# Optimization experiments

Measured on AMD Instinct MI355X. Metric: run time of the kernel, lower is better.

Reference implementation:

```python
import jax, jax.numpy as jnp
import numpy as np
import math

N, C, E, K_TOP = 4096, 256, 131072, 32
NEG_SLOPE = 0.2  # GATConv default negative_slope


def _mlp(x, w1, b1, w2, b2):
    # Linear -> relu -> Linear (dropout is identity in eval mode)
    return jax.nn.relu(x @ w1 + b1) @ w2 + b2


def _gat_alpha(x, w, a_src, a_dst, src, dst, n):
    # PyG GATConv attention coefficients (heads=1), softmax over incoming edges per dst
    h = x @ w                                                   # [N,C]
    logits = jax.nn.leaky_relu((h @ a_src)[src] + (h @ a_dst)[dst], NEG_SLOPE)  # [E]
    m = jnp.full((n,), -jnp.inf, dtype=logits.dtype).at[dst].max(logits)
    e = jnp.exp(logits - m[dst])
    s = jax.ops.segment_sum(e, dst, num_segments=n)
    return e / s[dst]                                           # [E]


def _mha_w(x, wq, bq, wk, bk):
    # nn.MultiheadAttention attention weights, heads=1, unbatched [N,C] input
    q = x @ wq + bq
    k = x @ wk + bk
    return jax.nn.softmax((q @ k.T) * (1.0 / math.sqrt(C)), axis=-1)  # [N,N]


def _forward(ae, pe, se,
             ae_w1, ae_b1, ae_w2, ae_b2,
             pe_w1, pe_b1, pe_w2, pe_b2,
             se_w1, se_b1, se_w2, se_b2,
             ae_gw, ae_as, ae_ad,
             pe_gw, pe_as, pe_ad,
             se_gw, se_as, se_ad,
             ae_wq, ae_bq, ae_wk, ae_bk,
             pe_wq, pe_bq, pe_wk, pe_bk,
             se_wq, se_bq, se_wk, se_bk,
             a_l, b_l, c_l, a_g, b_g, c_g,
             w_local, w_global,
             edge_index, K):
    n = ae.shape[0]
    ae = _mlp(ae, ae_w1, ae_b1, ae_w2, ae_b2)
    pe = _mlp(pe, pe_w1, pe_b1, pe_w2, pe_b2)
    se = _mlp(se, se_w1, se_b1, se_w2, se_b2)

    src, dst = edge_index[0], edge_index[1]

    # ---- local branch: fused GAT attention coeffs -> weighted mean aggregation ----
    pa = _gat_alpha(pe, pe_gw, pe_as, pe_ad, src, dst, n)
    sa = _gat_alpha(se, se_gw, se_as, se_ad, src, dst, n)
    aa = _gat_alpha(ae, ae_gw, ae_as, ae_ad, src, dst, n)
    local_attn = a_l * pa + b_l * sa + c_l * aa                 # [E]
    msg = local_attn[:, None] * ae[src]                         # [E,C]
    summ = jax.ops.segment_sum(msg, dst, num_segments=n)
    cnt = jax.ops.segment_sum(jnp.ones((src.shape[0],), msg.dtype), dst, num_segments=n)
    out_local = summ / jnp.maximum(cnt, 1.0)[:, None]           # mean aggr

    # ---- global branch: dense self-attn maps + adj masking + per-column top-K ----
    pw = _mha_w(pe, pe_wq, pe_bq, pe_wk, pe_bk)                 # [N,N]
    sw = _mha_w(se, se_wq, se_bq, se_wk, se_bk)
    aw = _mha_w(ae, ae_wq, ae_bq, ae_wk, ae_bk)
    sample_attn = a_g * pw + b_g * sw
    adj = jnp.zeros((n, n), sample_attn.dtype).at[src, dst].add(1.0)
    sample_attn = jnp.where(adj > 0, jnp.zeros((), sample_attn.dtype), sample_attn)
    # torch topk(dim=1) on [1,N,N] == top-K along axis 0 (per column) of [N,N]
    _, idx = jax.lax.top_k(sample_attn.T, K)                    # [N,K] row indices per column
    maskT = jnp.zeros((n, n), sample_attn.dtype).at[jnp.arange(n)[:, None], idx].set(1.0)
    mask = maskT.T
    g_attn = (0.5 * a_g + 0.5 * b_g) * (sample_attn * mask) + c_g * (aw * mask)
    col = jnp.sum(g_attn, axis=0)                               # column sums (torch dim=1 on [1,N,N])
    g_attn = g_attn / col[None, :]
    out_global = g_attn @ ae                                    # [N,C]

    return out_local @ w_local + out_global @ w_global


def setup_inputs() -> dict:
    key = jax.random.key(0)
    it = iter(jax.random.split(key, 64))
    g = lambda shape, s=0.06: jax.random.normal(next(it), shape, dtype=jnp.float32) * s
    inp = {"ae": g((N, C), 1.0), "pe": g((N, C), 1.0), "se": g((N, C), 1.0)}
    for p in ("ae", "pe", "se"):
        inp[p + "_w1"] = g((C, 2 * C)); inp[p + "_b1"] = jnp.zeros((2 * C,), jnp.float32)
        inp[p + "_w2"] = g((2 * C, C)); inp[p + "_b2"] = jnp.zeros((C,), jnp.float32)
        inp[p + "_gw"] = g((C, C)); inp[p + "_as"] = g((C,)); inp[p + "_ad"] = g((C,))
        inp[p + "_wq"] = g((C, C)); inp[p + "_bq"] = jnp.zeros((C,), jnp.float32)
        inp[p + "_wk"] = g((C, C)); inp[p + "_bk"] = jnp.zeros((C,), jnp.float32)
    for s in ("a_l", "b_l", "c_l", "a_g", "b_g", "c_g"):
        inp[s] = jnp.float32(0.33)
    inp["w_local"] = g((C, C))
    inp["w_global"] = g((C, C))
    inp["edge_index"] = jax.random.randint(next(it), (2, E), 0, N, dtype=jnp.int32)
    inp["K"] = K_TOP
    return inp


def reference(ae, pe, se,
              ae_w1, ae_b1, ae_w2, ae_b2,
              pe_w1, pe_b1, pe_w2, pe_b2,
              se_w1, se_b1, se_w2, se_b2,
              ae_gw, ae_as, ae_ad,
              pe_gw, pe_as, pe_ad,
              se_gw, se_as, se_ad,
              ae_wq, ae_bq, ae_wk, ae_bk,
              pe_wq, pe_bq, pe_wk, pe_bk,
              se_wq, se_bq, se_wk, se_bk,
              a_l, b_l, c_l, a_g, b_g, c_g,
              w_local, w_global,
              edge_index, K):
    return _forward(ae, pe, se,
                    ae_w1, ae_b1, ae_w2, ae_b2,
                    pe_w1, pe_b1, pe_w2, pe_b2,
                    se_w1, se_b1, se_w2, se_b2,
                    ae_gw, ae_as, ae_ad,
                    pe_gw, pe_as, pe_ad,
                    se_gw, se_as, se_ad,
                    ae_wq, ae_bq, ae_wk, ae_bk,
                    pe_wq, pe_bq, pe_wk, pe_bk,
                    se_wq, se_bq, se_wk, se_bk,
                    a_l, b_l, c_l, a_g, b_g, c_g,
                    w_local, w_global,
                    edge_index, K)
```

## Files before the change

kernel.cpp:

```cpp
#include <hip/hip_runtime.h>

#define NN 4096
#define CC 256
#define EE 131072
#define KT 32

typedef unsigned short ushort_t;
typedef __attribute__((ext_vector_type(8))) short short8;
typedef __attribute__((ext_vector_type(4))) float float4v;

__device__ __forceinline__ ushort_t f2bf(float x) {
    union { float f; unsigned u; } a; a.f = x;
    unsigned r = (a.u + 0x7FFF + ((a.u >> 16) & 1)) >> 16;
    return (ushort_t)r;
}
__device__ __forceinline__ float bf2f(ushort_t b) {
    union { float f; unsigned u; } a; a.u = ((unsigned)b) << 16;
    return a.f;
}

constexpr size_t OFF_EPT  = 0;
constexpr size_t OFF_EST  = OFF_EPT + 16777216;
constexpr size_t OFF_LP   = OFF_EST + 16777216;
constexpr size_t OFF_LS   = OFF_LP + 4096;
constexpr size_t OFF_LA   = OFF_LS + 4096;
constexpr size_t OFF_ECNT = OFF_LA + 4096;
constexpr size_t OFF_GCNT = OFF_ECNT + 4096;
constexpr size_t OFF_ADJ  = OFF_GCNT + 4096;
constexpr size_t ZERO_END = OFF_ADJ + 524288;
constexpr size_t OFF_XM   = ZERO_END;
constexpr size_t OFF_QK   = OFF_XM + 3*1048576;
constexpr size_t OFF_WEXP = OFF_QK + 6*1048576;
constexpr size_t OFF_HS   = OFF_WEXP + 3*131072;
constexpr size_t OFF_HD   = OFF_HS + 12288;
constexpr size_t OFF_WSD  = OFF_HD + 12288;
constexpr size_t OFF_TKI  = OFF_WSD + 1536;
constexpr size_t OFF_TKV  = OFF_TKI + 131072;
constexpr size_t OFF_GN   = OFF_TKV + 131072;
constexpr size_t OFF_EOFF = OFF_GN + 131072;
constexpr size_t OFF_ECUR = OFF_EOFF + 4097;
constexpr size_t OFF_ELST = OFF_ECUR + 4096;
constexpr size_t OFF_GOFF = OFF_ELST + 131072;
constexpr size_t OFF_GCUR = OFF_GOFF + 4097;
constexpr size_t OFF_GLST = OFF_GCUR + 4096;
constexpr size_t OFF_WLT  = OFF_GLST + 131072;
constexpr size_t WS_FLOATS = OFF_WLT + 131072;

constexpr size_t SH_XINH = 0;
constexpr size_t SH_XINL = 3145728;
constexpr size_t SH_HIDH = 6291456;
constexpr size_t SH_HIDL = 12582912;
constexpr size_t SH_XMH  = 18874368;
constexpr size_t SH_XML  = 22020096;
constexpr size_t SH_WT   = 25165824;
constexpr size_t WT_BR   = 786432;

struct TArgs {
    const float* s[14]; ushort_t* h[14]; ushort_t* l[14];
    int nshift[14]; int total[14]; int kstride[14]; int koff[14];
};

__global__ __launch_bounds__(256)
void wtrans_k(TArgs a)
{
    int z = blockIdx.z;
    int idx = blockIdx.x * 256 + threadIdx.x;
    if (idx >= a.total[z]) return;
    int n = idx & ((1 << a.nshift[z]) - 1);
    int k = idx >> a.nshift[z];
    float v = a.s[z][idx];
    ushort_t hh = f2bf(v);
    size_t o = (size_t)n * a.kstride[z] + a.koff[z] + k;
    a.h[z][o] = hh;
    a.l[z][o] = f2bf(v - bf2f(hh));
}

__global__ __launch_bounds__(256)
void split3_k(const float* s0, const float* s1, const float* s2,
              ushort_t* hb, ushort_t* lb, size_t nper)
{
    int z = blockIdx.z;
    const float* s = (z == 0) ? s0 : (z == 1) ? s1 : s2;
    ushort_t* h = hb + (size_t)z * nper;
    ushort_t* l = lb + (size_t)z * nper;
    size_t i = (size_t)(blockIdx.x * 256 + threadIdx.x) * 4;
    float4 v = *(const float4*)(s + i);
    ushort_t h0 = f2bf(v.x), h1 = f2bf(v.y), h2 = f2bf(v.z), h3 = f2bf(v.w);
    ushort_t l0 = f2bf(v.x - bf2f(h0)), l1 = f2bf(v.y - bf2f(h1));
    ushort_t l2 = f2bf(v.z - bf2f(h2)), l3 = f2bf(v.w - bf2f(h3));
    uint2 hw, lw;
    hw.x = (unsigned)h0 | ((unsigned)h1 << 16); hw.y = (unsigned)h2 | ((unsigned)h3 << 16);
    lw.x = (unsigned)l0 | ((unsigned)l1 << 16); lw.y = (unsigned)l2 | ((unsigned)l3 << 16);
    *(uint2*)(h + i) = hw;
    *(uint2*)(l + i) = lw;
}

struct MArgs {
    const ushort_t* Ah[6]; const ushort_t* Al[6];
    const ushort_t* Bh[6]; const ushort_t* Bl[6];
    const float* bias[6];
    float* Cf[6]; ushort_t* Ch[6]; ushort_t* Cl[6];
};

template<int RELU>
__global__ __launch_bounds__(256)
void mgemm_k(MArgs a, int N, int K)
{
    __shared__ ushort_t SA[2][64 * 32];
    __shared__ ushort_t SB[2][64 * 32];

    const int z = blockIdx.z;
    const int t = threadIdx.x, wave = t >> 6, lane = t & 63;
    const int wi = wave & 1, wj = wave >> 1;
    const int lrow = lane & 15, lquad = lane >> 4;

    const ushort_t* src = (wave == 0) ? a.Ah[z] : (wave == 1) ? a.Al[z]
                        : (wave == 2) ? a.Bh[z] : a.Bl[z];
    ushort_t* dst = (wave == 0) ? &SA[0][0] : (wave == 1) ? &SA[1][0]
                  : (wave == 2) ? &SB[0][0] : &SB[1][0];
    const int rbase = ((wave < 2) ? blockIdx.x : blockIdx.y) * 64;
    const int sr = lane >> 2, sq = lane & 3;
    const int gsq = sq ^ ((sr >> 1) & 3);

    float4v acc[2][2] = {};

    for (int k0 = 0; k0 < K; k0 += 32) {
        #pragma unroll
        for (int it = 0; it < 4; ++it) {
            const ushort_t* g = src + (size_t)(rbase + it * 16 + sr) * K + k0 + gsq * 8;
            __builtin_amdgcn_global_load_lds(
                (const __attribute__((address_space(1))) void*)g,
                (__attribute__((address_space(3))) void*)(dst + it * 512),
                16, 0, 0);
        }
        __syncthreads();

        short8 fAh[2], fAl[2], fBh[2], fBl[2];
        #pragma unroll
        for (int mt = 0; mt < 2; ++mt) {
            int ra = wi * 32 + mt * 16 + lrow;
            int ca = (lquad ^ ((ra >> 1) & 3)) * 8;
            fAh[mt] = *(const short8*)&SA[0][ra * 32 + ca];
            fAl[mt] = *(const short8*)&SA[1][ra * 32 + ca];
        }
        #pragma unroll
        for (int nt = 0; nt < 2; ++nt) {
            int rb = wj * 32 + nt * 16 + lrow;
            int cb = (lquad ^ ((rb >> 1) & 3)) * 8;
            fBh[nt] = *(const short8*)&SB[0][rb * 32 + cb];
            fBl[nt] = *(const short8*)&SB[1][rb * 32 + cb];
        }
        #pragma unroll
        for (int mt = 0; mt < 2; ++mt)
            #pragma unroll
            for (int nt = 0; nt < 2; ++nt) {
                acc[mt][nt] = __builtin_amdgcn_mfma_f32_16x16x32_bf16(fAh[mt], fBh[nt], acc[mt][nt], 0, 0, 0);
                acc[mt][nt] = __builtin_amdgcn_mfma_f32_16x16x32_bf16(fAh[mt], fBl[nt], acc[mt][nt], 0, 0, 0);
                acc[mt][nt] = __builtin_amdgcn_mfma_f32_16x16x32_bf16(fAl[mt], fBh[nt], acc[mt][nt], 0, 0, 0);
            }
        __syncthreads();
    }

    const float* bias = a.bias[z];
    float* Cf = a.Cf[z];
    ushort_t* Ch = a.Ch[z]; ushort_t* Cl = a.Cl[z];
    const int i0w = blockIdx.x * 64 + wi * 32, j0w = blockIdx.y * 64 + wj * 32;
    #pragma unroll
    for (int mt = 0; mt < 2; ++mt) {
        const int ib = i0w + mt * 16 + lquad * 4;
        #pragma unroll
        for (int nt = 0; nt < 2; ++nt) {
            const int j = j0w + nt * 16 + lrow;
            float bj = bias ? bias[j] : 0.f;
            #pragma unroll
            for (int r = 0; r < 4; ++r) {
                float v = acc[mt][nt][r] + bj;
                if (RELU) v = fmaxf(v, 0.f);
                if (Cf) Cf[(size_t)(ib + r) * N + j] = v;
                if (Ch) {
                    ushort_t h = f2bf(v);
                    Ch[(size_t)(ib + r) * N + j] = h;
                    Cl[(size_t)(ib + r) * N + j] = f2bf(v - bf2f(h));
                }
            }
        }
    }
}

struct QArgs {
    const ushort_t* qh[3]; const ushort_t* ql[3];
    const ushort_t* kh[3]; const ushort_t* kl[3];
    float* ept[3]; float* rs[3];
};

__global__ __launch_bounds__(256)
void qk_mfma_k(QArgs a, float scale)
{
    __shared__ ushort_t SA[2][128 * 32];
    __shared__ ushort_t SB[2][128 * 32];

    const int z = blockIdx.z;
    const int t = threadIdx.x;
    const int wave = t >> 6, lane = t & 63;
    const int wi = wave & 1, wj = wave >> 1;
    const int i0w = blockIdx.x * 128 + wi * 64;
    const int j0w = blockIdx.y * 128 + wj * 64;
    const int lrow = lane & 15, lquad = lane >> 4;

    const ushort_t* src = (wave == 0) ? a.qh[z] : (wave == 1) ? a.ql[z]
                        : (wave == 2) ? a.kh[z] : a.kl[z];
    ushort_t* dst = (wave == 0) ? &SA[0][0] : (wave == 1) ? &SA[1][0]
                  : (wave == 2) ? &SB[0][0] : &SB[1][0];
    const int rbase = (wave < 2) ? blockIdx.x * 128 : blockIdx.y * 128;
    const int sr = lane >> 2, sq = lane & 3;
    const int gsq = sq ^ ((sr >> 1) & 3);

    float4v acc[4][4] = {};

    for (int k0 = 0; k0 < CC; k0 += 32) {
        #pragma unroll
        for (int it = 0; it < 8; ++it) {
            const ushort_t* g = src + (size_t)(rbase + it * 16 + sr) * CC + k0 + gsq * 8;
            __builtin_amdgcn_global_load_lds(
                (const __attribute__((address_space(1))) void*)g,
                (__attribute__((address_space(3))) void*)(dst + it * 512),
                16, 0, 0);
        }
        __syncthreads();

        short8 Ah[4], Al[4], Bh[4], Bl[4];
        #pragma unroll
        for (int mt = 0; mt < 4; ++mt) {
            int ra = wi * 64 + mt * 16 + lrow;
            int ca = (lquad ^ ((ra >> 1) & 3)) * 8;
            Ah[mt] = *(const short8*)&SA[0][ra * 32 + ca];
            Al[mt] = *(const short8*)&SA[1][ra * 32 + ca];
        }
        #pragma unroll
        for (int nt = 0; nt < 4; ++nt) {
            int rb = wj * 64 + nt * 16 + lrow;
            int cb = (lquad ^ ((rb >> 1) & 3)) * 8;
            Bh[nt] = *(const short8*)&SB[0][rb * 32 + cb];
            Bl[nt] = *(const short8*)&SB[1][rb * 32 + cb];
        }
        #pragma unroll
        for (int mt = 0; mt < 4; ++mt)
            #pragma unroll
            for (int nt = 0; nt < 4; ++nt) {
                acc[mt][nt] = __builtin_amdgcn_mfma_f32_16x16x32_bf16(Ah[mt], Bh[nt], acc[mt][nt], 0, 0, 0);
                acc[mt][nt] = __builtin_amdgcn_mfma_f32_16x16x32_bf16(Ah[mt], Bl[nt], acc[mt][nt], 0, 0, 0);
                acc[mt][nt] = __builtin_amdgcn_mfma_f32_16x16x32_bf16(Al[mt], Bh[nt], acc[mt][nt], 0, 0, 0);
            }
        __syncthreads();
    }

    float* ept = a.ept[z];
    float* rowsum = a.rs[z];
    #pragma unroll
    for (int mt = 0; mt < 4; ++mt) {
        const int ib = i0w + mt * 16 + lquad * 4;
        float part[4] = {0.f, 0.f, 0.f, 0.f};
        #pragma unroll
        for (int nt = 0; nt < 4; ++nt) {
            const int j = j0w + nt * 16 + lrow;
            float e0 = expf(acc[mt][nt][0] * scale);
            float e1 = expf(acc[mt][nt][1] * scale);
            float e2 = expf(acc[mt][nt][2] * scale);
            float e3 = expf(acc[mt][nt][3] * scale);
            part[0] += e0; part[1] += e1; part[2] += e2; part[3] += e3;
            if (ept)
                *(float4*)&ept[(size_t)j * NN + ib] = make_float4(e0, e1, e2, e3);
        }
        #pragma unroll
        for (int r = 0; r < 4; ++r) {
            float p = part[r];
            p += __shfl_xor(p, 1, 64);
            p += __shfl_xor(p, 2, 64);
            p += __shfl_xor(p, 4, 64);
            p += __shfl_xor(p, 8, 64);
            if (lrow == 0) atomicAdd(&rowsum[ib + r], p);
        }
    }
}

__global__ void invrows_k(float* __restrict__ lp, float* __restrict__ ls,
                          const float* agp, const float* bgp)
{
    int i = blockIdx.x * 256 + threadIdx.x;
    lp[i] = (*agp) / lp[i];
    ls[i] = (*bgp) / ls[i];
}

__global__ __launch_bounds__(256)
void gatvec_k(const float* g0, const float* g1, const float* g2,
              const float* v0, const float* v1, const float* v2,
              const float* v3, const float* v4, const float* v5,
              float* __restrict__ wsd)
{
    int b = blockIdx.x;
    const float* gw = (b < 2) ? g0 : (b < 4) ? g1 : g2;
    const float* av = (b == 0) ? v0 : (b == 1) ? v1 : (b == 2) ? v2
                    : (b == 3) ? v3 : (b == 4) ? v4 : v5;
    int tdx = threadIdx.x;
    float s = 0.f;
    for (int c = 0; c < CC; ++c) s += gw[(size_t)tdx * CC + c] * av[c];
    wsd[b * 256 + tdx] = s;
}

__global__ __launch_bounds__(256)
void hshd_k(const float* __restrict__ Xp, const float* __restrict__ Xs,
            const float* __restrict__ Xa, const float* __restrict__ wsd,
            float* __restrict__ hs, float* __restrict__ hd)
{
    int b = blockIdx.y, row = blockIdx.x, t = threadIdx.x;
    const float* X = (b == 0) ? Xp : (b == 1) ? Xs : Xa;
    float x = X[(size_t)row * CC + t];
    float p1 = x * wsd[b * 512 + t];
    float p2 = x * wsd[b * 512 + 256 + t];
    for (int off = 32; off; off >>= 1) {
        p1 += __shfl_down(p1, off, 64);
        p2 += __shfl_down(p2, off, 64);
    }
    __shared__ float s1[4], s2[4];
    if ((t & 63) == 0) { s1[t >> 6] = p1; s2[t >> 6] = p2; }
    __syncthreads();
    if (t == 0) {
        hs[b * NN + row] = s1[0] + s1[1] + s1[2] + s1[3];
        hd[b * NN + row] = s2[0] + s2[1] + s2[2] + s2[3];
    }
}

__global__ __launch_bounds__(256)
void edge_k(const int* __restrict__ ei, const float* __restrict__ hs,
            const float* __restrict__ hd, float* __restrict__ wexp,
            unsigned* __restrict__ bits, int* __restrict__ cnt)
{
    int e = blockIdx.x * 256 + threadIdx.x;
    int s = ei[e], d = ei[EE + e];
    #pragma unroll
    for (int b = 0; b < 3; ++b) {
        float l = hs[b * NN + s] + hd[b * NN + d];
        l = (l > 0.f) ? l : 0.2f * l;
        wexp[(size_t)b * EE + e] = expf(l);
    }
    size_t lin = (size_t)d * NN + s;
    atomicOr(&bits[lin >> 5], 1u << (lin & 31));
    atomicAdd(&cnt[d], 1);
}

__global__ void gcount_k(const int* __restrict__ tki, int* __restrict__ cnt)
{
    int p = blockIdx.x * 256 + threadIdx.x;
    atomicAdd(&cnt[tki[p]], 1);
}

__global__ __launch_bounds__(256)
void prefix_k(const int* __restrict__ cnt, int* __restrict__ off, int* __restrict__ cur)
{
    __shared__ int part[257];
    int t = threadIdx.x;
    int loc[16]; int s = 0;
    #pragma unroll
    for (int u = 0; u < 16; ++u) { loc[u] = s; s += cnt[t * 16 + u]; }
    part[t + 1] = s;
    if (t == 0) part[0] = 0;
    __syncthreads();
    if (t == 0) for (int i = 1; i <= 256; ++i) part[i] += part[i - 1];
    __syncthreads();
    int b = part[t];
    #pragma unroll
    for (int u = 0; u < 16; ++u) { off[t * 16 + u] = b + loc[u]; cur[t * 16 + u] = b + loc[u]; }
    if (t == 255) off[4096] = part[256];
}

__global__ void efill_k(const int* __restrict__ ei, int* __restrict__ cur,
                        int* __restrict__ lst)
{
    int e = blockIdx.x * 256 + threadIdx.x;
    int p = atomicAdd(&cur[ei[EE + e]], 1);
    lst[p] = e;
}

__global__ void gfill_k(const int* __restrict__ tki, int* __restrict__ cur,
                        int* __restrict__ lst)
{
    int p = blockIdx.x * 256 + threadIdx.x;
    int q = atomicAdd(&cur[tki[p]], 1);
    lst[q] = p;
}

__global__ __launch_bounds__(256)
void topk_k(const float* __restrict__ EPT, const float* __restrict__ EST,
            const float* __restrict__ ivp, const float* __restrict__ ivs,
            const unsigned* __restrict__ adjbits,
            int* __restrict__ tki, float* __restrict__ tkv)
{
    __shared__ unsigned lst[4][KT];
    const int j = blockIdx.x, t = threadIdx.x;
    const int w = t >> 6, lane = t & 63;
    const size_t base = (size_t)j * NN;

    unsigned keys[16], kmax = 0;
    #pragma unroll
    for (int u = 0; u < 16; ++u) {
        int i = w * 1024 + u * 64 + lane;
        float v = EPT[base + i] * ivp[i] + EST[base + i] * ivs[i];
        if ((adjbits[(base + i) >> 5] >> (i & 31)) & 1u) v = 0.f;
        union { float f; unsigned u32; } cv; cv.f = v;
        unsigned k = (cv.u32 & 0xFFFFFC00u) | (unsigned)(1023 - (i & 1023));
        keys[u] = k;
        kmax = k > kmax ? k : kmax;
    }

    for (int r = 0; r < KT; ++r) {
        unsigned k = kmax;
        #pragma unroll
        for (int off = 1; off < 64; off <<= 1) {
            unsigned o = __shfl_xor(k, off, 64);
            k = o > k ? o : k;
        }
        if (lane == 0) lst[w][r] = k;
        if (kmax == k) {
            kmax = 0;
            #pragma unroll
            for (int u = 0; u < 16; ++u) {
                if (keys[u] == k) keys[u] = 0;
                kmax = keys[u] > kmax ? keys[u] : kmax;
            }
        }
    }
    __syncthreads();

    if (t == 0) {
        unsigned h0 = lst[0][0], h1 = lst[1][0], h2 = lst[2][0], h3 = lst[3][0];
        int p0 = 0, p1 = 0, p2 = 0, p3 = 0;
        for (int r = 0; r < KT; ++r) {
            unsigned m01 = h0 > h1 ? h0 : h1;
            unsigned m23 = h2 > h3 ? h2 : h3;
            unsigned m = m01 > m23 ? m01 : m23;
            int wsel;
            if      (m == h0) { wsel = 0; ++p0; h0 = (p0 < KT) ? lst[0][p0] : 0; }
            else if (m == h1) { wsel = 1; ++p1; h1 = (p1 < KT) ? lst[1][p1] : 0; }
            else if (m == h2) { wsel = 2; ++p2; h2 = (p2 < KT) ? lst[2][p2] : 0; }
            else              { wsel = 3; ++p3; h3 = (p3 < KT) ? lst[3][p3] : 0; }
            union { unsigned u32; float f; } cv; cv.u32 = m & 0xFFFFFC00u;
            tkv[j * KT + r] = cv.f;
            tki[j * KT + r] = wsel * 1024 + 1023 - (int)(m & 0x3FFu);
        }
    }
}

__global__ __launch_bounds__(256)
void awcol_k(const ushort_t* __restrict__ qh, const ushort_t* __restrict__ ql,
             const ushort_t* __restrict__ kh, const ushort_t* __restrict__ kl,
             const float* __restrict__ La, const int* __restrict__ tki,
             const float* __restrict__ tkv,
             const float* agp, const float* bgp, const float* cgp,
             float* __restrict__ gn)
{
    __shared__ float kj[CC];
    __shared__ float gv[KT];
    __shared__ float cs_sh;
    int j = blockIdx.x, t = threadIdx.x;
    kj[t] = bf2f(kh[(size_t)j * CC + t]) + bf2f(kl[(size_t)j * CC + t]);
    __syncthreads();
    float hg = 0.5f * (*agp) + 0.5f * (*bgp), cg = *cgp;
    int wv = t >> 6, ln = t & 63;
    for (int k = wv; k < KT; k += 4) {
        int i = tki[j * KT + k];
        float p = 0.f;
        #pragma unroll
        for (int u = 0; u < 4; ++u) {
            int c = ln + u * 64;
            float q = bf2f(qh[(size_t)i * CC + c]) + bf2f(ql[(size_t)i * CC + c]);
            p += q * kj[c];
        }
        for (int off = 32; off; off >>= 1) p += __shfl_down(p, off, 64);
        if (ln == 0) {
            float aw = expf(p * 0.0625f) / La[i];
            gv[k] = hg * tkv[j * KT + k] + cg * aw;
        }
    }
    __syncthreads();
    if (t == 0) { float cs = 0.f; for (int k = 0; k < KT; ++k) cs += gv[k]; cs_sh = cs; }
    __syncthreads();
    if (t < KT) gn[j * KT + t] = gv[t] / cs_sh;
}

__global__ __launch_bounds__(256)
void lgather_k(const int* __restrict__ ei, const int* __restrict__ eoff,
               const int* __restrict__ elst,
               const float* __restrict__ wexp,
               const float* __restrict__ aem,
               const float* alp, const float* blp, const float* clp,
               ushort_t* __restrict__ outch, ushort_t* __restrict__ outcl)
{
    int wv = threadIdx.x >> 6, ln = threadIdx.x & 63;
    int d = blockIdx.x * 4 + wv;
    int beg = eoff[d], end = eoff[d + 1];

    float s1 = 0.f, s2 = 0.f, s3 = 0.f;
    for (int c = beg + ln; c < end; c += 64) {
        int e = elst[c];
        s1 += wexp[e];
        s2 += wexp[EE + e];
        s3 += wexp[2 * (size_t)EE + e];
    }
    #pragma unroll
    for (int off = 1; off < 64; off <<= 1) {
        s1 += __shfl_xor(s1, off, 64);
        s2 += __shfl_xor(s2, off, 64);
        s3 += __shfl_xor(s3, off, 64);
    }
    float i0 = (*alp) / s1, i1 = (*blp) / s2, i2 = (*clp) / s3;

    float4 acc = {0.f, 0.f, 0.f, 0.f};
    for (int c = beg; c < end; c += 64) {
        int n = min(64, end - c);
        int s = 0; float la = 0.f;
        if (ln < n) {
            int e = elst[c + ln];
            s = ei[e];
            la = i0 * wexp[e] + i1 * wexp[EE + e] + i2 * wexp[2 * (size_t)EE + e];
        }
        for (int u = 0; u < n; ++u) {
            float lau = __shfl(la, u, 64);
            int   su  = __shfl(s, u, 64);
            const float4 v = *(const float4*)&aem[(size_t)su * CC + ln * 4];
            acc.x += lau * v.x; acc.y += lau * v.y;
            acc.z += lau * v.z; acc.w += lau * v.w;
        }
    }
    float inv = 1.f / fmaxf((float)(end - beg), 1.f);
    acc.x *= inv; acc.y *= inv; acc.z *= inv; acc.w *= inv;
    ushort_t h0 = f2bf(acc.x), h1 = f2bf(acc.y), h2 = f2bf(acc.z), h3 = f2bf(acc.w);
    uint2 hw, lw;
    hw.x = (unsigned)h0 | ((unsigned)h1 << 16); hw.y = (unsigned)h2 | ((unsigned)h3 << 16);
    lw.x = (unsigned)f2bf(acc.x - bf2f(h0)) | ((unsigned)f2bf(acc.y - bf2f(h1)) << 16);
    lw.y = (unsigned)f2bf(acc.z - bf2f(h2)) | ((unsigned)f2bf(acc.w - bf2f(h3)) << 16);
    *(uint2*)&outch[(size_t)d * 512 + ln * 4] = hw;
    *(uint2*)&outcl[(size_t)d * 512 + ln * 4] = lw;
}

__global__ __launch_bounds__(256)
void ggather_k(const int* __restrict__ goff, const int* __restrict__ glst,
               const float* __restrict__ gn, const float* __restrict__ aem,
               ushort_t* __restrict__ outch, ushort_t* __restrict__ outcl)
{
    int wv = threadIdx.x >> 6, ln = threadIdx.x & 63;
    int i = blockIdx.x * 4 + wv;
    int beg = goff[i], end = goff[i + 1];
    float4 acc = {0.f, 0.f, 0.f, 0.f};
    for (int c = beg; c < end; c += 64) {
        int n = min(64, end - c);
        int j = 0; float g = 0.f;
        if (ln < n) {
            int p = glst[c + ln];
            j = p >> 5;
            g = gn[p];
        }
        for (int u = 0; u < n; ++u) {
            float gu = __shfl(g, u, 64);
            int   ju = __shfl(j, u, 64);
            const float4 v = *(const float4*)&aem[(size_t)ju * CC + ln * 4];
            acc.x += gu * v.x; acc.y += gu * v.y;
            acc.z += gu * v.z; acc.w += gu * v.w;
        }
    }
    ushort_t h0 = f2bf(acc.x), h1 = f2bf(acc.y), h2 = f2bf(acc.z), h3 = f2bf(acc.w);
    uint2 hw, lw;
    hw.x = (unsigned)h0 | ((unsigned)h1 << 16); hw.y = (unsigned)h2 | ((unsigned)h3 << 16);
    lw.x = (unsigned)f2bf(acc.x - bf2f(h0)) | ((unsigned)f2bf(acc.y - bf2f(h1)) << 16);
    lw.y = (unsigned)f2bf(acc.z - bf2f(h2)) | ((unsigned)f2bf(acc.w - bf2f(h3)) << 16);
    *(uint2*)&outch[(size_t)i * 512 + 256 + ln * 4] = hw;
    *(uint2*)&outcl[(size_t)i * 512 + 256 + ln * 4] = lw;
}

__global__ void diag_k(float* out, float v) { out[0] = v; }

extern "C" void kernel_launch(void* const* d_in, const int* in_sizes, int n_in,
                              void* d_out, int out_size, void* d_ws, size_t ws_size,
                              hipStream_t stream)
{
    (void)in_sizes; (void)n_in; (void)out_size;

    if (ws_size < WS_FLOATS * sizeof(float)) {
        diag_k<<<1, 1, 0, stream>>>((float*)d_out, (float)(ws_size >> 20));
        return;
    }

    float* W = (float*)d_ws;
    float* EPT = W + OFF_EPT;  float* EST = W + OFF_EST;
    float* LP = W + OFF_LP;    float* LS = W + OFF_LS;   float* LA = W + OFF_LA;
    int* ECNT = (int*)(W + OFF_ECNT);
    int* GCNT = (int*)(W + OFF_GCNT);
    unsigned* ADJ = (unsigned*)(W + OFF_ADJ);
    float* XM = W + OFF_XM;
    ushort_t* QKS = (ushort_t*)(W + OFF_QK);
    float* WEXP = W + OFF_WEXP;
    float* HS = W + OFF_HS;    float* HD = W + OFF_HD;   float* WSD = W + OFF_WSD;
    int*   TKI = (int*)(W + OFF_TKI);
    float* TKV = W + OFF_TKV;  float* GN = W + OFF_GN;
    int* EOFF = (int*)(W + OFF_EOFF); int* ECUR = (int*)(W + OFF_ECUR);
    int* ELST = (int*)(W + OFF_ELST);
    int* GOFF = (int*)(W + OFF_GOFF); int* GCUR = (int*)(W + OFF_GCUR);
    int* GLST = (int*)(W + OFF_GLST);

    ushort_t* PRO = (ushort_t*)EPT;
    ushort_t* EPI = (ushort_t*)EST;
    ushort_t* WLT = (ushort_t*)(W + OFF_WLT);

    ushort_t* XINH = PRO + SH_XINH; ushort_t* XINL = PRO + SH_XINL;
    ushort_t* HIDH = PRO + SH_HIDH; ushort_t* HIDL = PRO + SH_HIDL;
    ushort_t* XMH  = PRO + SH_XMH;  ushort_t* XML  = PRO + SH_XML;

    auto W1T = [&](int b, int hl) { return PRO + SH_WT + (size_t)b * WT_BR + hl * 131072; };
    auto W2T = [&](int b, int hl) { return PRO + SH_WT + (size_t)b * WT_BR + 262144 + hl * 131072; };
    auto WQT = [&](int b, int hl) { return PRO + SH_WT + (size_t)b * WT_BR + 524288 + hl * 65536; };
    auto WKT = [&](int b, int hl) { return PRO + SH_WT + (size_t)b * WT_BR + 655360 + hl * 65536; };
    ushort_t* WCT_H = WLT;
    ushort_t* WCT_L = WLT + 131072;
    ushort_t* OUTCH = EPI;
    ushort_t* OUTCL = EPI + 2097152;

    auto QHp = [&](int b) { return QKS + (size_t)(b * 4 + 0) * 1048576; };
    auto QLp = [&](int b) { return QKS + (size_t)(b * 4 + 1) * 1048576; };
    auto KHp = [&](int b) { return QKS + (size_t)(b * 4 + 2) * 1048576; };
    auto KLp = [&](int b) { return QKS + (size_t)(b * 4 + 3) * 1048576; };

    const float* Xin[3] = {(const float*)d_in[1], (const float*)d_in[2], (const float*)d_in[0]};
    const int base_idx[3] = {14, 25, 3};
    const float *w1[3], *b1[3], *w2[3], *b2[3], *gw[3], *asv[3], *adv[3], *wq[3], *bq[3], *wk[3], *bk[3];
    for (int b = 0; b < 3; ++b) {
        int o = base_idx[b];
        w1[b] = (const float*)d_in[o + 0]; b1[b] = (const float*)d_in[o + 1];
        w2[b] = (const float*)d_in[o + 2]; b2[b] = (const float*)d_in[o + 3];
        gw[b] = (const float*)d_in[o + 4]; asv[b] = (const float*)d_in[o + 5];
        adv[b] = (const float*)d_in[o + 6];
        wq[b] = (const float*)d_in[o + 7]; bq[b] = (const float*)d_in[o + 8];
        wk[b] = (const float*)d_in[o + 9]; bk[b] = (const float*)d_in[o + 10];
    }
    const float* al = (const float*)d_in[36]; const float* bl = (const float*)d_in[37];
    const float* cl = (const float*)d_in[38];
    const float* ag = (const float*)d_in[39]; const float* bg = (const float*)d_in[40];
    const float* cg = (const float*)d_in[41];
    const float* wloc = (const float*)d_in[42];
    const float* wglb = (const float*)d_in[43];
    const int* ei = (const int*)d_in[44];

    dim3 blk(256);

    hipMemsetAsync(LP, 0, (ZERO_END - OFF_LP) * sizeof(float), stream);

    {
        TArgs a{};
        for (int b = 0; b < 3; ++b) {
            a.s[b] = w1[b]; a.h[b] = W1T(b, 0); a.l[b] = W1T(b, 1);
            a.nshift[b] = 9; a.total[b] = 131072; a.kstride[b] = 256; a.koff[b] = 0;
            a.s[3 + b] = w2[b]; a.h[3 + b] = W2T(b, 0); a.l[3 + b] = W2T(b, 1);
            a.nshift[3 + b] = 8; a.total[3 + b] = 131072; a.kstride[3 + b] = 512; a.koff[3 + b] = 0;
            a.s[6 + b] = wq[b]; a.h[6 + b] = WQT(b, 0); a.l[6 + b] = WQT(b, 1);
            a.nshift[6 + b] = 8; a.total[6 + b] = 65536; a.kstride[6 + b] = 256; a.koff[6 + b] = 0;
            a.s[9 + b] = wk[b]; a.h[9 + b] = WKT(b, 0); a.l[9 + b] = WKT(b, 1);
            a.nshift[9 + b] = 8; a.total[9 + b] = 65536; a.kstride[9 + b] = 256; a.koff[9 + b] = 0;
        }
        a.s[12] = wloc; a.h[12] = WCT_H; a.l[12] = WCT_L;
        a.nshift[12] = 8; a.total[12] = 65536; a.kstride[12] = 512; a.koff[12] = 0;
        a.s[13] = wglb; a.h[13] = WCT_H; a.l[13] = WCT_L;
        a.nshift[13] = 8; a.total[13] = 65536; a.kstride[13] = 512; a.koff[13] = 256;
        wtrans_k<<<dim3(512, 1, 14), blk, 0, stream>>>(a);
    }

    split3_k<<<dim3(1024, 1, 3), blk, 0, stream>>>(Xin[0], Xin[1], Xin[2], XINH, XINL, 1048576);

    {
        MArgs a{};
        for (int b = 0; b < 3; ++b) {
            a.Ah[b] = XINH + (size_t)b * 1048576; a.Al[b] = XINL + (size_t)b * 1048576;
            a.Bh[b] = W1T(b, 0); a.Bl[b] = W1T(b, 1); a.bias[b] = b1[b];
            a.Cf[b] = nullptr;
            a.Ch[b] = HIDH + (size_t)b * 2097152; a.Cl[b] = HIDL + (size_t)b * 2097152;
        }
        mgemm_k<1><<<dim3(64, 8, 3), blk, 0, stream>>>(a, 512, 256);
    }
    {
        MArgs a{};
        for (int b = 0; b < 3; ++b) {
            a.Ah[b] = HIDH + (size_t)b * 2097152; a.Al[b] = HIDL + (size_t)b * 2097152;
            a.Bh[b] = W2T(b, 0); a.Bl[b] = W2T(b, 1); a.bias[b] = b2[b];
            a.Cf[b] = XM + (size_t)b * 1048576;
            a.Ch[b] = XMH + (size_t)b * 1048576; a.Cl[b] = XML + (size_t)b * 1048576;
        }
        mgemm_k<0><<<dim3(64, 4, 3), blk, 0, stream>>>(a, 256, 512);
    }

    gatvec_k<<<6, blk, 0, stream>>>(gw[0], gw[1], gw[2],
                                    asv[0], adv[0], asv[1], adv[1], asv[2], adv[2], WSD);
    hshd_k<<<dim3(NN, 3), blk, 0, stream>>>(XM, XM + 1048576, XM + 2 * 1048576, WSD, HS, HD);
    edge_k<<<EE / 256, blk, 0, stream>>>(ei, HS, HD, WEXP, ADJ, ECNT);

    prefix_k<<<1, blk, 0, stream>>>(ECNT, EOFF, ECUR);
    efill_k<<<EE / 256, blk, 0, stream>>>(ei, ECUR, ELST);

    {
        MArgs a{};
        for (int b = 0; b < 3; ++b) {
            a.Ah[b] = XMH + (size_t)b * 1048576; a.Al[b] = XML + (size_t)b * 1048576;
            a.Bh[b] = WQT(b, 0); a.Bl[b] = WQT(b, 1); a.bias[b] = bq[b];
            a.Cf[b] = nullptr; a.Ch[b] = QHp(b); a.Cl[b] = QLp(b);
            a.Ah[3 + b] = a.Ah[b]; a.Al[3 + b] = a.Al[b];
            a.Bh[3 + b] = WKT(b, 0); a.Bl[3 + b] = WKT(b, 1); a.bias[3 + b] = bk[b];
            a.Cf[3 + b] = nullptr; a.Ch[3 + b] = KHp(b); a.Cl[3 + b] = KLp(b);
        }
        mgemm_k<0><<<dim3(64, 4, 6), blk, 0, stream>>>(a, 256, 256);
    }

    {
        QArgs a{};
        for (int b = 0; b < 3; ++b) {
            a.qh[b] = QHp(b); a.ql[b] = QLp(b); a.kh[b] = KHp(b); a.kl[b] = KLp(b);
        }
        a.ept[0] = EPT; a.rs[0] = LP;
        a.ept[1] = EST; a.rs[1] = LS;
        a.ept[2] = nullptr; a.rs[2] = LA;
        qk_mfma_k<<<dim3(32, 32, 3), blk, 0, stream>>>(a, 0.0625f);
    }

    invrows_k<<<16, blk, 0, stream>>>(LP, LS, ag, bg);

    topk_k<<<NN, blk, 0, stream>>>(EPT, EST, LP, LS, ADJ, TKI, TKV);

    gcount_k<<<(NN * KT) / 256, blk, 0, stream>>>(TKI, GCNT);
    prefix_k<<<1, blk, 0, stream>>>(GCNT, GOFF, GCUR);
    gfill_k<<<(NN * KT) / 256, blk, 0, stream>>>(TKI, GCUR, GLST);

    awcol_k<<<NN, blk, 0, stream>>>(QHp(2), QLp(2), KHp(2), KLp(2), LA,
                                    TKI, TKV, ag, bg, cg, GN);

    lgather_k<<<NN / 4, blk, 0, stream>>>(ei, EOFF, ELST, WEXP,
                                          XM + 2 * 1048576, al, bl, cl, OUTCH, OUTCL);
    ggather_k<<<NN / 4, blk, 0, stream>>>(GOFF, GLST, GN, XM + 2 * 1048576, OUTCH, OUTCL);

    {
        MArgs a{};
        a.Ah[0] = OUTCH; a.Al[0] = OUTCL;
        a.Bh[0] = WCT_H; a.Bl[0] = WCT_L; a.bias[0] = nullptr;
        a.Cf[0] = (float*)d_out; a.Ch[0] = nullptr; a.Cl[0] = nullptr;
        mgemm_k<0><<<dim3(64, 4, 1), blk, 0, stream>>>(a, 256, 512);
    }
}
```

Measured before the change: 568.7 us.

## Enlarge GEMM tiles, fuse gathers, use fast exp, rework topk index tracking

The split-bf16 MFMA GEMM now computes a 128x64 tile per block, with each wave owning 32 rows, and the grids are halved to match. This improves reuse of B operands but halves the number of blocks. The local and global gather kernels are merged into one launch, and the inner accumulation loop is unrolled by 4 to issue more loads in flight. expf is replaced with a hardware exp2-based approximation in several kernels. Top-k now keeps full float keys with separate index arrays instead of packing the index into the low mantissa bits, which changes the selection logic and its tie handling.

```diff
diff --git a/kernel.cpp b/kernel.cpp
--- a/kernel.cpp
+++ b/kernel.cpp
@@ -17,6 +17,13 @@
 __device__ __forceinline__ float bf2f(ushort_t b) {
     union { float f; unsigned u; } a; a.u = ((unsigned)b) << 16;
     return a.f;
+}
+__device__ __forceinline__ float fexp(float x) {
+#if __has_builtin(__builtin_amdgcn_exp2f)
+    return __builtin_amdgcn_exp2f(x * 1.4426950408889634f);
+#else
+    return exp2f(x * 1.4426950408889634f);
+#endif
 }
 
 constexpr size_t OFF_EPT  = 0;
@@ -106,46 +113,56 @@
 __global__ __launch_bounds__(256)
 void mgemm_k(MArgs a, int N, int K)
 {
-    __shared__ ushort_t SA[2][64 * 32];
+    __shared__ ushort_t SA[2][128 * 32];
     __shared__ ushort_t SB[2][64 * 32];
 
     const int z = blockIdx.z;
     const int t = threadIdx.x, wave = t >> 6, lane = t & 63;
-    const int wi = wave & 1, wj = wave >> 1;
     const int lrow = lane & 15, lquad = lane >> 4;
 
     const ushort_t* src = (wave == 0) ? a.Ah[z] : (wave == 1) ? a.Al[z]
                         : (wave == 2) ? a.Bh[z] : a.Bl[z];
     ushort_t* dst = (wave == 0) ? &SA[0][0] : (wave == 1) ? &SA[1][0]
                   : (wave == 2) ? &SB[0][0] : &SB[1][0];
-    const int rbase = ((wave < 2) ? blockIdx.x : blockIdx.y) * 64;
+    const int rbase = (wave < 2) ? blockIdx.x * 128 : blockIdx.y * 64;
     const int sr = lane >> 2, sq = lane & 3;
     const int gsq = sq ^ ((sr >> 1) & 3);
 
-    float4v acc[2][2] = {};
+    float4v acc[2][4] = {};
 
     for (int k0 = 0; k0 < K; k0 += 32) {
-        #pragma unroll
-        for (int it = 0; it < 4; ++it) {
-            const ushort_t* g = src + (size_t)(rbase + it * 16 + sr) * K + k0 + gsq * 8;
-            __builtin_amdgcn_global_load_lds(
-                (const __attribute__((address_space(1))) void*)g,
-                (__attribute__((address_space(3))) void*)(dst + it * 512),
-                16, 0, 0);
+        if (wave < 2) {
+            #pragma unroll
+            for (int it = 0; it < 8; ++it) {
+                const ushort_t* g = src + (size_t)(rbase + it * 16 + sr) * K + k0 + gsq * 8;
+                __builtin_amdgcn_global_load_lds(
+                    (const __attribute__((address_space(1))) void*)g,
+                    (__attribute__((address_space(3))) void*)(dst + it * 512),
+                    16, 0, 0);
+            }
+        } else {
+            #pragma unroll
+            for (int it = 0; it < 4; ++it) {
+                const ushort_t* g = src + (size_t)(rbase + it * 16 + sr) * K + k0 + gsq * 8;
+                __builtin_amdgcn_global_load_lds(
+                    (const __attribute__((address_space(1))) void*)g,
+                    (__attribute__((address_space(3))) void*)(dst + it * 512),
+                    16, 0, 0);
+            }
         }
         __syncthreads();
 
-        short8 fAh[2], fAl[2], fBh[2], fBl[2];
+        short8 fAh[2], fAl[2], fBh[4], fBl[4];
         #pragma unroll
         for (int mt = 0; mt < 2; ++mt) {
-            int ra = wi * 32 + mt * 16 + lrow;
+            int ra = wave * 32 + mt * 16 + lrow;
             int ca = (lquad ^ ((ra >> 1) & 3)) * 8;
             fAh[mt] = *(const short8*)&SA[0][ra * 32 + ca];
             fAl[mt] = *(const short8*)&SA[1][ra * 32 + ca];
         }
         #pragma unroll
-        for (int nt = 0; nt < 2; ++nt) {
-            int rb = wj * 32 + nt * 16 + lrow;
+        for (int nt = 0; nt < 4; ++nt) {
+            int rb = nt * 16 + lrow;
             int cb = (lquad ^ ((rb >> 1) & 3)) * 8;
             fBh[nt] = *(const short8*)&SB[0][rb * 32 + cb];
             fBl[nt] = *(const short8*)&SB[1][rb * 32 + cb];
@@ -153,7 +170,7 @@
         #pragma unroll
         for (int mt = 0; mt < 2; ++mt)
             #pragma unroll
-            for (int nt = 0; nt < 2; ++nt) {
+            for (int nt = 0; nt < 4; ++nt) {
                 acc[mt][nt] = __builtin_amdgcn_mfma_f32_16x16x32_bf16(fAh[mt], fBh[nt], acc[mt][nt], 0, 0, 0);
                 acc[mt][nt] = __builtin_amdgcn_mfma_f32_16x16x32_bf16(fAh[mt], fBl[nt], acc[mt][nt], 0, 0, 0);
                 acc[mt][nt] = __builtin_amdgcn_mfma_f32_16x16x32_bf16(fAl[mt], fBh[nt], acc[mt][nt], 0, 0, 0);
@@ -164,12 +181,12 @@
     const float* bias = a.bias[z];
     float* Cf = a.Cf[z];
     ushort_t* Ch = a.Ch[z]; ushort_t* Cl = a.Cl[z];
-    const int i0w = blockIdx.x * 64 + wi * 32, j0w = blockIdx.y * 64 + wj * 32;
+    const int i0w = blockIdx.x * 128 + wave * 32, j0w = blockIdx.y * 64;
     #pragma unroll
     for (int mt = 0; mt < 2; ++mt) {
         const int ib = i0w + mt * 16 + lquad * 4;
         #pragma unroll
-        for (int nt = 0; nt < 2; ++nt) {
+        for (int nt = 0; nt < 4; ++nt) {
             const int j = j0w + nt * 16 + lrow;
             float bj = bias ? bias[j] : 0.f;
             #pragma unroll
@@ -263,10 +280,10 @@
         #pragma unroll
         for (int nt = 0; nt < 4; ++nt) {
             const int j = j0w + nt * 16 + lrow;
-            float e0 = expf(acc[mt][nt][0] * scale);
-            float e1 = expf(acc[mt][nt][1] * scale);
-            float e2 = expf(acc[mt][nt][2] * scale);
-            float e3 = expf(acc[mt][nt][3] * scale);
+            float e0 = fexp(acc[mt][nt][0] * scale);
+            float e1 = fexp(acc[mt][nt][1] * scale);
+            float e2 = fexp(acc[mt][nt][2] * scale);
+            float e3 = fexp(acc[mt][nt][3] * scale);
             part[0] += e0; part[1] += e1; part[2] += e2; part[3] += e3;
             if (ept)
                 *(float4*)&ept[(size_t)j * NN + ib] = make_float4(e0, e1, e2, e3);
@@ -341,7 +358,7 @@
     for (int b = 0; b < 3; ++b) {
         float l = hs[b * NN + s] + hd[b * NN + d];
         l = (l > 0.f) ? l : 0.2f * l;
-        wexp[(size_t)b * EE + e] = expf(l);
+        wexp[(size_t)b * EE + e] = fexp(l);
     }
     size_t lin = (size_t)d * NN + s;
     atomicOr(&bits[lin >> 5], 1u << (lin & 31));
@@ -395,7 +412,8 @@
             const unsigned* __restrict__ adjbits,
             int* __restrict__ tki, float* __restrict__ tkv)
 {
-    __shared__ unsigned lst[4][KT];
+    __shared__ unsigned lv[4][KT];
+    __shared__ int      li[4][KT];
     const int j = blockIdx.x, t = threadIdx.x;
     const int w = t >> 6, lane = t & 63;
     const size_t base = (size_t)j * NN;
@@ -407,9 +425,8 @@
         float v = EPT[base + i] * ivp[i] + EST[base + i] * ivs[i];
         if ((adjbits[(base + i) >> 5] >> (i & 31)) & 1u) v = 0.f;
         union { float f; unsigned u32; } cv; cv.f = v;
-        unsigned k = (cv.u32 & 0xFFFFFC00u) | (unsigned)(1023 - (i & 1023));
-        keys[u] = k;
-        kmax = k > kmax ? k : kmax;
+        keys[u] = cv.u32;
+        kmax = keys[u] > kmax ? keys[u] : kmax;
     }
 
     for (int r = 0; r < KT; ++r) {
@@ -419,33 +436,40 @@
             unsigned o = __shfl_xor(k, off, 64);
             k = o > k ? o : k;
         }
-        if (lane == 0) lst[w][r] = k;
-        if (kmax == k) {
+        if (lane == 0) { lv[w][r] = k; li[w][r] = w * 1024; }
+        if (kmax == k && k != 0) {
+            bool done = false;
+            #pragma unroll
+            for (int u = 0; u < 16; ++u) {
+                if (!done && keys[u] == k) {
+                    li[w][r] = w * 1024 + u * 64 + lane;
+                    keys[u] = 0;
+                    done = true;
+                }
+            }
             kmax = 0;
             #pragma unroll
-            for (int u = 0; u < 16; ++u) {
-                if (keys[u] == k) keys[u] = 0;
-                kmax = keys[u] > kmax ? keys[u] : kmax;
-            }
+            for (int u = 0; u < 16; ++u) kmax = keys[u] > kmax ? keys[u] : kmax;
         }
     }
     __syncthreads();
 
     if (t == 0) {
-        unsigned h0 = lst[0][0], h1 = lst[1][0], h2 = lst[2][0], h3 = lst[3][0];
-        int p0 = 0, p1 = 0, p2 = 0, p3 = 0;
+        unsigned hv[4] = {lv[0][0], lv[1][0], lv[2][0], lv[3][0]};
+        int      hi_[4] = {li[0][0], li[1][0], li[2][0], li[3][0]};
+        int      pp[4] = {0, 0, 0, 0};
         for (int r = 0; r < KT; ++r) {
-            unsigned m01 = h0 > h1 ? h0 : h1;
-            unsigned m23 = h2 > h3 ? h2 : h3;
-            unsigned m = m01 > m23 ? m01 : m23;
-            int wsel;
-            if      (m == h0) { wsel = 0; ++p0; h0 = (p0 < KT) ? lst[0][p0] : 0; }
-            else if (m == h1) { wsel = 1; ++p1; h1 = (p1 < KT) ? lst[1][p1] : 0; }
-            else if (m == h2) { wsel = 2; ++p2; h2 = (p2 < KT) ? lst[2][p2] : 0; }
-            else              { wsel = 3; ++p3; h3 = (p3 < KT) ? lst[3][p3] : 0; }
-            union { unsigned u32; float f; } cv; cv.u32 = m & 0xFFFFFC00u;
+            int best = 0;
+            #pragma unroll
+            for (int wsel = 1; wsel < 4; ++wsel)
+                if (hv[wsel] > hv[best] || (hv[wsel] == hv[best] && hi_[wsel] < hi_[best]))
+                    best = wsel;
+            union { unsigned u32; float f; } cv; cv.u32 = hv[best];
             tkv[j * KT + r] = cv.f;
-            tki[j * KT + r] = wsel * 1024 + 1023 - (int)(m & 0x3FFu);
+            tki[j * KT + r] = hi_[best];
+            int p = ++pp[best];
+            hv[best]  = (p < KT) ? lv[best][p] : 0u;
+            hi_[best] = (p < KT) ? li[best][p] : 0x7FFFFFFF;
         }
     }
 }
@@ -477,7 +501,7 @@
         }
         for (int off = 32; off; off >>= 1) p += __shfl_down(p, off, 64);
         if (ln == 0) {
-            float aw = expf(p * 0.0625f) / La[i];
+            float aw = fexp(p * 0.0625f) / La[i];
             gv[k] = hg * tkv[j * KT + k] + cg * aw;
         }
     }
@@ -487,93 +511,104 @@
     if (t < KT) gn[j * KT + t] = gv[t] / cs_sh;
 }
 
-__global__ __launch_bounds__(256)
-void lgather_k(const int* __restrict__ ei, const int* __restrict__ eoff,
-               const int* __restrict__ elst,
-               const float* __restrict__ wexp,
-               const float* __restrict__ aem,
-               const float* alp, const float* blp, const float* clp,
-               ushort_t* __restrict__ outch, ushort_t* __restrict__ outcl)
+__device__ __forceinline__ void gather_accum(const float* __restrict__ aem, int ln, int n,
+                                             float la, int s, float4& acc)
+{
+    int u = 0;
+    for (; u + 4 <= n; u += 4) {
+        float l0 = __shfl(la, u, 64),     l1 = __shfl(la, u + 1, 64);
+        float l2 = __shfl(la, u + 2, 64), l3 = __shfl(la, u + 3, 64);
+        int   s0 = __shfl(s, u, 64),      s1 = __shfl(s, u + 1, 64);
+        int   s2 = __shfl(s, u + 2, 64),  s3 = __shfl(s, u + 3, 64);
+        const float4 v0 = *(const float4*)&aem[(size_t)s0 * CC + ln * 4];
+        const float4 v1 = *(const float4*)&aem[(size_t)s1 * CC + ln * 4];
+        const float4 v2 = *(const float4*)&aem[(size_t)s2 * CC + ln * 4];
+        const float4 v3 = *(const float4*)&aem[(size_t)s3 * CC + ln * 4];
+        acc.x += l0 * v0.x + l1 * v1.x + l2 * v2.x + l3 * v3.x;
+        acc.y += l0 * v0.y + l1 * v1.y + l2 * v2.y + l3 * v3.y;
+        acc.z += l0 * v0.z + l1 * v1.z + l2 * v2.z + l3 * v3.z;
+        acc.w += l0 * v0.w + l1 * v1.w + l2 * v2.w + l3 * v3.w;
+    }
+    for (; u < n; ++u) {
+        float lu = __shfl(la, u, 64);
+        int   su = __shfl(s, u, 64);
+        const float4 v = *(const float4*)&aem[(size_t)su * CC + ln * 4];
+        acc.x += lu * v.x; acc.y += lu * v.y;
+        acc.z += lu * v.z; acc.w += lu * v.w;
+    }
+}
+
+__global__ __launch_bounds__(256)
+void gather_k(const int* __restrict__ ei, const int* __restrict__ eoff,
+              const int* __restrict__ elst, const float* __restrict__ wexp,
+              const int* __restrict__ goff, const int* __restrict__ glst,
+              const float* __restrict__ gn, const float* __restrict__ aem,
+              const float* alp, const float* blp, const float* clp,
+              ushort_t* __restrict__ outch, ushort_t* __restrict__ outcl)
 {
     int wv = threadIdx.x >> 6, ln = threadIdx.x & 63;
-    int d = blockIdx.x * 4 + wv;
-    int beg = eoff[d], end = eoff[d + 1];
-
-    float s1 = 0.f, s2 = 0.f, s3 = 0.f;
-    for (int c = beg + ln; c < end; c += 64) {
-        int e = elst[c];
-        s1 += wexp[e];
-        s2 += wexp[EE + e];
-        s3 += wexp[2 * (size_t)EE + e];
-    }
-    #pragma unroll
-    for (int off = 1; off < 64; off <<= 1) {
-        s1 += __shfl_xor(s1, off, 64);
-        s2 += __shfl_xor(s2, off, 64);
-        s3 += __shfl_xor(s3, off, 64);
-    }
-    float i0 = (*alp) / s1, i1 = (*blp) / s2, i2 = (*clp) / s3;
-
     float4 acc = {0.f, 0.f, 0.f, 0.f};
-    for (int c = beg; c < end; c += 64) {
-        int n = min(64, end - c);
-        int s = 0; float la = 0.f;
-        if (ln < n) {
-            int e = elst[c + ln];
-            s = ei[e];
-            la = i0 * wexp[e] + i1 * wexp[EE + e] + i2 * wexp[2 * (size_t)EE + e];
-        }
-        for (int u = 0; u < n; ++u) {
-            float lau = __shfl(la, u, 64);
-            int   su  = __shfl(s, u, 64);
-            const float4 v = *(const float4*)&aem[(size_t)su * CC + ln * 4];
-            acc.x += lau * v.x; acc.y += lau * v.y;
-            acc.z += lau * v.z; acc.w += lau * v.w;
-        }
-    }
-    float inv = 1.f / fmaxf((float)(end - beg), 1.f);
-    acc.x *= inv; acc.y *= inv; acc.z *= inv; acc.w *= inv;
-    ushort_t h0 = f2bf(acc.x), h1 = f2bf(acc.y), h2 = f2bf(acc.z), h3 = f2bf(acc.w);
-    uint2 hw, lw;
-    hw.x = (unsigned)h0 | ((unsigned)h1 << 16); hw.y = (unsigned)h2 | ((unsigned)h3 << 16);
-    lw.x = (unsigned)f2bf(acc.x - bf2f(h0)) | ((unsigned)f2bf(acc.y - bf2f(h1)) << 16);
-    lw.y = (unsigned)f2bf(acc.z - bf2f(h2)) | ((unsigned)f2bf(acc.w - bf2f(h3)) << 16);
-    *(uint2*)&outch[(size_t)d * 512 + ln * 4] = hw;
-    *(uint2*)&outcl[(size_t)d * 512 + ln * 4] = lw;
-}
-
-__global__ __launch_bounds__(256)
-void ggather_k(const int* __restrict__ goff, const int* __restrict__ glst,
-               const float* __restrict__ gn, const float* __restrict__ aem,
-               ushort_t* __restrict__ outch, ushort_t* __restrict__ outcl)
-{
-    int wv = threadIdx.x >> 6, ln = threadIdx.x & 63;
-    int i = blockIdx.x * 4 + wv;
-    int beg = goff[i], end = goff[i + 1];
-    float4 acc = {0.f, 0.f, 0.f, 0.f};
-    for (int c = beg; c < end; c += 64) {
-        int n = min(64, end - c);
-        int j = 0; float g = 0.f;
-        if (ln < n) {
-            int p = glst[c + ln];
-            j = p >> 5;
-            g = gn[p];
-        }
-        for (int u = 0; u < n; ++u) {
-            float gu = __shfl(g, u, 64);
-            int   ju = __shfl(j, u, 64);
-            const float4 v = *(const float4*)&aem[(size_t)ju * CC + ln * 4];
-            acc.x += gu * v.x; acc.y += gu * v.y;
-            acc.z += gu * v.z; acc.w += gu * v.w;
-        }
-    }
-    ushort_t h0 = f2bf(acc.x), h1 = f2bf(acc.y), h2 = f2bf(acc.z), h3 = f2bf(acc.w);
-    uint2 hw, lw;
-    hw.x = (unsigned)h0 | ((unsigned)h1 << 16); hw.y = (unsigned)h2 | ((unsigned)h3 << 16);
-    lw.x = (unsigned)f2bf(acc.x - bf2f(h0)) | ((unsigned)f2bf(acc.y - bf2f(h1)) << 16);
-    lw.y = (unsigned)f2bf(acc.z - bf2f(h2)) | ((unsigned)f2bf(acc.w - bf2f(h3)) << 16);
-    *(uint2*)&outch[(size_t)i * 512 + 256 + ln * 4] = hw;
-    *(uint2*)&outcl[(size_t)i * 512 + 256 + ln * 4] = lw;
+
+    if (blockIdx.x < NN / 4) {
+        int d = blockIdx.x * 4 + wv;
+        int beg = eoff[d], end = eoff[d + 1];
+
+        float s1 = 0.f, s2 = 0.f, s3 = 0.f;
+        for (int c = beg + ln; c < end; c += 64) {
+            int e = elst[c];
+            s1 += wexp[e];
+            s2 += wexp[EE + e];
+            s3 += wexp[2 * (size_t)EE + e];
+        }
+        #pragma unroll
+        for (int off = 1; off < 64; off <<= 1) {
+            s1 += __shfl_xor(s1, off, 64);
+            s2 += __shfl_xor(s2, off, 64);
+            s3 += __shfl_xor(s3, off, 64);
+        }
+        float i0 = (*alp) / s1, i1 = (*blp) / s2, i2 = (*clp) / s3;
+
+        for (int c = beg; c < end; c += 64) {
+            int n = min(64, end - c);
+            int s = 0; float la = 0.f;
+            if (ln < n) {
+                int e = elst[c + ln];
+                s = ei[e];
+                la = i0 * wexp[e] + i1 * wexp[EE + e] + i2 * wexp[2 * (size_t)EE + e];
+            }
+            gather_accum(aem, ln, n, la, s, acc);
+        }
+        float inv = 1.f / fmaxf((float)(end - beg), 1.f);
+        acc.x *= inv; acc.y *= inv; acc.z *= inv; acc.w *= inv;
+
+        ushort_t h0 = f2bf(acc.x), h1 = f2bf(acc.y), h2 = f2bf(acc.z), h3 = f2bf(acc.w);
+        uint2 hw, lw;
+        hw.x = (unsigned)h0 | ((unsigned)h1 << 16); hw.y = (unsigned)h2 | ((unsigned)h3 << 16);
+        lw.x = (unsigned)f2bf(acc.x - bf2f(h0)) | ((unsigned)f2bf(acc.y - bf2f(h1)) << 16);
+        lw.y = (unsigned)f2bf(acc.z - bf2f(h2)) | ((unsigned)f2bf(acc.w - bf2f(h3)) << 16);
+        *(uint2*)&outch[(size_t)d * 512 + ln * 4] = hw;
+        *(uint2*)&outcl[(size_t)d * 512 + ln * 4] = lw;
+    } else {
+        int i = (blockIdx.x - NN / 4) * 4 + wv;
+        int beg = goff[i], end = goff[i + 1];
+        for (int c = beg; c < end; c += 64) {
+            int n = min(64, end - c);
+            int jcol = 0; float g = 0.f;
+            if (ln < n) {
+                int p = glst[c + ln];
+                jcol = p >> 5;
+                g = gn[p];
+            }
+            gather_accum(aem, ln, n, g, jcol, acc);
+        }
+        ushort_t h0 = f2bf(acc.x), h1 = f2bf(acc.y), h2 = f2bf(acc.z), h3 = f2bf(acc.w);
+        uint2 hw, lw;
+        hw.x = (unsigned)h0 | ((unsigned)h1 << 16); hw.y = (unsigned)h2 | ((unsigned)h3 << 16);
+        lw.x = (unsigned)f2bf(acc.x - bf2f(h0)) | ((unsigned)f2bf(acc.y - bf2f(h1)) << 16);
+        lw.y = (unsigned)f2bf(acc.z - bf2f(h2)) | ((unsigned)f2bf(acc.w - bf2f(h3)) << 16);
+        *(uint2*)&outch[(size_t)i * 512 + 256 + ln * 4] = hw;
+        *(uint2*)&outcl[(size_t)i * 512 + 256 + ln * 4] = lw;
+    }
 }
 
 __global__ void diag_k(float* out, float v) { out[0] = v; }
@@ -681,7 +716,7 @@
             a.Cf[b] = nullptr;
             a.Ch[b] = HIDH + (size_t)b * 2097152; a.Cl[b] = HIDL + (size_t)b * 2097152;
         }
-        mgemm_k<1><<<dim3(64, 8, 3), blk, 0, stream>>>(a, 512, 256);
+        mgemm_k<1><<<dim3(32, 8, 3), blk, 0, stream>>>(a, 512, 256);
     }
     {
         MArgs a{};
@@ -691,7 +726,7 @@
             a.Cf[b] = XM + (size_t)b * 1048576;
             a.Ch[b] = XMH + (size_t)b * 1048576; a.Cl[b] = XML + (size_t)b * 1048576;
         }
-        mgemm_k<0><<<dim3(64, 4, 3), blk, 0, stream>>>(a, 256, 512);
+        mgemm_k<0><<<dim3(32, 4, 3), blk, 0, stream>>>(a, 256, 512);
     }
 
     gatvec_k<<<6, blk, 0, stream>>>(gw[0], gw[1], gw[2],
@@ -712,7 +747,7 @@
             a.Bh[3 + b] = WKT(b, 0); a.Bl[3 + b] = WKT(b, 1); a.bias[3 + b] = bk[b];
             a.Cf[3 + b] = nullptr; a.Ch[3 + b] = KHp(b); a.Cl[3 + b] = KLp(b);
         }
-        mgemm_k<0><<<dim3(64, 4, 6), blk, 0, stream>>>(a, 256, 256);
+        mgemm_k<0><<<dim3(32, 4, 6), blk, 0, stream>>>(a, 256, 256);
     }
 
     {
@@ -737,15 +772,14 @@
     awcol_k<<<NN, blk, 0, stream>>>(QHp(2), QLp(2), KHp(2), KLp(2), LA,
                                     TKI, TKV, ag, bg, cg, GN);
 
-    lgather_k<<<NN / 4, blk, 0, stream>>>(ei, EOFF, ELST, WEXP,
-                                          XM + 2 * 1048576, al, bl, cl, OUTCH, OUTCL);
-    ggather_k<<<NN / 4, blk, 0, stream>>>(GOFF, GLST, GN, XM + 2 * 1048576, OUTCH, OUTCL);
+    gather_k<<<NN / 2, blk, 0, stream>>>(ei, EOFF, ELST, WEXP, GOFF, GLST, GN,
+                                         XM + 2 * 1048576, al, bl, cl, OUTCH, OUTCL);
 
     {
         MArgs a{};
         a.Ah[0] = OUTCH; a.Al[0] = OUTCL;
         a.Bh[0] = WCT_H; a.Bl[0] = WCT_L; a.bias[0] = nullptr;
         a.Cf[0] = (float*)d_out; a.Ch[0] = nullptr; a.Cl[0] = nullptr;
-        mgemm_k<0><<<dim3(64, 4, 1), blk, 0, stream>>>(a, 256, 512);
-    }
-}
+        mgemm_k<0><<<dim3(32, 4, 1), blk, 0, stream>>>(a, 256, 512);
+    }
+}
```

Result: slower. 616.2 us (+8.4%).
